# Kernel tuning notes

Hardware: AMD Instinct MI355X
Metric: run time of the kernel (lower is better)

The kernel has to match this reference:

```python
import math
import jax, jax.numpy as jnp
import numpy as np

# --- Cayley-Dickson octonion structure constants: e_i * e_j = sign * e_{i XOR j} ---
def _cd_tables(levels=3):
    idx = np.array([[0]]); sgn = np.array([[1]])
    for _ in range(levels):
        n = idx.shape[0]; N = 2 * n
        I = np.zeros((N, N), np.int64); S = np.zeros((N, N), np.int64)
        cj = lambda j: 1 if j == 0 else -1  # conj sign of basis element j
        for i in range(n):
            for j in range(n):
                I[i, j] = idx[i, j];             S[i, j] = sgn[i, j]
                I[i, n + j] = n + idx[j, i];     S[i, n + j] = sgn[j, i]
                I[n + i, j] = n + idx[i, j];     S[n + i, j] = sgn[i, j] * cj(j)
                I[n + i, n + j] = idx[j, i];     S[n + i, n + j] = -cj(j) * sgn[j, i]
        idx, sgn = I, S
    return idx, sgn

_OIDX, _OSGN = _cd_tables()
# Octonion-structured linear: out_i = sum_j SIGN[i,j] * x_j @ W[WIDX[i,j]], WIDX[i,j]=i^j
_WIDX = np.array([[i ^ j for j in range(8)] for i in range(8)], np.int64)
_SIGN = np.array([[_OSGN[j, i ^ j] for j in range(8)] for i in range(8)], np.float32)


def _oct_linear(x, W):
    # x: [B,T,C], W: [8, C/8, C/8]
    B, T, C = x.shape
    Cp = C // 8
    parts = x.reshape(B, T, 8, Cp)
    Weff = jnp.asarray(_SIGN)[:, :, None, None] * W[jnp.asarray(_WIDX)]  # [8,8,Cp,Cp]
    return jnp.einsum('btjp,ijpq->btiq', parts, Weff).reshape(B, T, C)


def _rope(x, cos, sin):
    # x: [B,T,H,D]; consecutive channel pairs form complex numbers
    B, T, H, D = x.shape
    xr = x.reshape(B, T, H, D // 2, 2)
    xe, xo = xr[..., 0], xr[..., 1]
    c = cos[None, :, None, :]
    s = sin[None, :, None, :]
    return jnp.stack([xe * c - xo * s, xe * s + xo * c], axis=-1).reshape(B, T, H, D)


def _forward(x, Wq, Wk, Wv, Wo, mixer_W, mixer_beta, freqs_cos, freqs_sin):
    B, T, C = x.shape
    H = 32; D = C // H
    q = _oct_linear(x, Wq).reshape(B, T, H, D)
    k = _oct_linear(x, Wk).reshape(B, T, H, D)
    v = _oct_linear(x, Wv).reshape(B, T, H, D)
    q = _rope(q, freqs_cos, freqs_sin)
    k = _rope(k, freqs_cos, freqs_sin)
    q = q.transpose(0, 2, 1, 3)  # [B,H,T,D]
    k = k.transpose(0, 2, 1, 3)
    v = v.transpose(0, 2, 1, 3)
    scores = jnp.einsum('bhqd,bhkd->bhqk', q, k) / jnp.sqrt(jnp.float32(D))
    mask = jnp.tril(jnp.ones((T, T), bool))
    scores = jnp.where(mask, scores, jnp.finfo(scores.dtype).min)
    y = jnp.einsum('bhqk,bhkd->bhqd', jax.nn.softmax(scores, axis=-1), v)  # [B,H,T,D]
    # octonion head mixing in groups of 8 heads
    G = H // 8
    yg = y.reshape(B, G, 8, T, D)
    Weff = jnp.asarray(_SIGN)[:, :, None, None] * mixer_W[jnp.asarray(_WIDX)]  # [8,8,D,D]
    mixed = jnp.einsum('bgjtd,ijde->bgite', yg, Weff) * mixer_beta
    y = mixed.reshape(B, H, T, D).transpose(0, 2, 1, 3).reshape(B, T, C)
    return _oct_linear(y, Wo)


def setup_inputs() -> dict:
    key = jax.random.key(0)
    ks = jax.random.split(key, 8)
    B, T, C, H = 1, 2048, 4096, 32
    D = C // H; Cp = C // 8
    x = jax.random.normal(ks[0], (B, T, C), jnp.float32)
    Wq = jax.random.normal(ks[1], (8, Cp, Cp), jnp.float32) * 0.02
    Wk = jax.random.normal(ks[2], (8, Cp, Cp), jnp.float32) * 0.02
    Wv = jax.random.normal(ks[3], (8, Cp, Cp), jnp.float32) * 0.02
    Wo = jax.random.normal(ks[4], (8, Cp, Cp), jnp.float32) * 0.02
    mixer_W = jax.random.normal(ks[5], (8, D, D), jnp.float32) * 0.02
    mixer_beta = jnp.ones((D,), jnp.float32) * np.float32(math.sqrt(3.0 / (2.0 * D)))
    half = D // 2
    inv = 1.0 / (10000.0 ** (np.arange(half) * 2.0 / D))
    ang = np.arange(T)[:, None] * inv[None, :]
    freqs_cos = jnp.asarray(np.cos(ang), jnp.float32)
    freqs_sin = jnp.asarray(np.sin(ang), jnp.float32)
    return dict(x=x, Wq=Wq, Wk=Wk, Wv=Wv, Wo=Wo, mixer_W=mixer_W,
                mixer_beta=mixer_beta, freqs_cos=freqs_cos, freqs_sin=freqs_sin)


def reference(x, Wq, Wk, Wv, Wo, mixer_W, mixer_beta, freqs_cos, freqs_sin):
    return _forward(x, Wq, Wk, Wv, Wo, mixer_W, mixer_beta, freqs_cos, freqs_sin)
```

## Files before the change

kernel.cpp:

```cpp
#include <hip/hip_runtime.h>

typedef float f32x4 __attribute__((ext_vector_type(4)));
typedef __bf16 bf16x8 __attribute__((ext_vector_type(8)));
typedef unsigned short u16;
typedef u16 u16x8 __attribute__((ext_vector_type(8)));

__constant__ float c_osgn[64] = {
  1, 1, 1, 1, 1, 1, 1, 1,
  1,-1, 1,-1, 1,-1,-1, 1,
  1,-1,-1, 1, 1, 1,-1,-1,
  1, 1,-1,-1, 1,-1, 1,-1,
  1,-1,-1,-1,-1, 1, 1, 1,
  1, 1,-1, 1,-1,-1,-1, 1,
  1, 1, 1,-1,-1, 1,-1,-1,
  1,-1, 1, 1,-1,-1, 1,-1
};

__device__ __forceinline__ u16 f2bf(float f) {
  union { float f; unsigned u; } v; v.f = f;
  unsigned u = v.u;
  return (u16)((u + 0x7fffu + ((u >> 16) & 1u)) >> 16);
}
__device__ __forceinline__ float bf2f(u16 h) {
  union { unsigned u; float f; } v; v.u = ((unsigned)h) << 16;
  return v.f;
}

typedef const __attribute__((address_space(1))) void* as1cv;
typedef __attribute__((address_space(3))) void* as3v;
__device__ __forceinline__ void load16_lds(const void* g, void* l) {
  __builtin_amdgcn_global_load_lds((as1cv)g, (as3v)l, 16, 0, 0);
}

__global__ void conv_f32_bf16_vec(const float* __restrict__ src, u16* __restrict__ dst) {
  int i = blockIdx.x * 256 + threadIdx.x;
  float4 v = ((const float4*)src)[i];
  ushort4 o; o.x = f2bf(v.x); o.y = f2bf(v.y); o.z = f2bf(v.z); o.w = f2bf(v.w);
  ((ushort4*)dst)[i] = o;
}

__global__ __launch_bounds__(256) void transpose_w2(const float* __restrict__ W,
                                                    u16* __restrict__ Wt) {
  __shared__ float t[64][65];
  const int w = blockIdx.z, p0 = blockIdx.y * 64, q0 = blockIdx.x * 64;
  const float* src = W + ((long)w * 512 + p0) * 512 + q0;
  const int tid = threadIdx.x;
  const int r = tid >> 2, c0 = (tid & 3) * 16;
#pragma unroll
  for (int j = 0; j < 4; j++) {
    float4 v = *(const float4*)(src + (long)r * 512 + c0 + j * 4);
    t[r][c0 + j * 4 + 0] = v.x; t[r][c0 + j * 4 + 1] = v.y;
    t[r][c0 + j * 4 + 2] = v.z; t[r][c0 + j * 4 + 3] = v.w;
  }
  __syncthreads();
  u16* dst = Wt + ((long)w * 512 + q0) * 512 + p0;
#pragma unroll
  for (int j = 0; j < 2; j++) {
    u16x8 o;
#pragma unroll
    for (int k = 0; k < 8; k++) o[k] = f2bf(t[c0 + j * 8 + k][r]);
    *(u16x8*)(dst + (long)r * 512 + c0 + j * 8) = o;
  }
}

__global__ void transpose_wm(const float* __restrict__ W, const float* __restrict__ beta,
                             u16* __restrict__ Wt) {
  int idx = blockIdx.x * 256 + threadIdx.x;
  int w = idx >> 14, rem = idx & 16383;
  int e = rem >> 7, d = rem & 127;
  Wt[(w << 14) + (e << 7) + d] = f2bf(W[(w << 14) + (d << 7) + e] * beta[e]);
}

template <typename OUT_T>
__global__ __launch_bounds__(512, 2) void oct_gemm2(
    const u16* __restrict__ A, const u16* __restrict__ WtB, OUT_T* __restrict__ Cout,
    int K, int lda, int ldo, long wslab, long oslab)
{
  __shared__ u16 As[2][256][64];
  __shared__ u16 Bs[2][128][64];
  const int NT = K >> 6;

  const int nwg = gridDim.x * gridDim.y;
  const int lin = blockIdx.y * gridDim.x + blockIdx.x;
  const int swz = (lin & 7) * (nwg >> 3) + (lin >> 3);
  const int bx = swz % gridDim.x, by = swz / gridDim.x;

  const int nglob = bx * 128;
  const int z = nglob >> 12;
  const int np = nglob & 4095;
  const int bi = np >> 9;
  const int nsub = np & 511;
  const int bm = by * 256;
  const u16* Wt = WtB + (long)z * wslab;
  OUT_T* outp = Cout + (long)z * oslab;

  const int tid = threadIdx.x;
  const int lane = tid & 63, w = tid >> 6;
  const int l15 = lane & 15, lg = lane >> 4;
  const int wm = w >> 1, wn = w & 1;
  const int srow = lane >> 3;
  const int sgr  = (lane & 7) ^ srow;

  f32x4 acc[4][4];
#pragma unroll
  for (int a = 0; a < 4; a++)
#pragma unroll
    for (int b = 0; b < 4; b++) acc[a][b] = f32x4{0.f, 0.f, 0.f, 0.f};

  auto stage = [&](int t, int buf) {
    const int k0 = t << 6;
    const int widx = bi ^ (k0 >> 9);
    const int kl = k0 & 511;
    const u16* Wsrc = Wt + (long)widx * 262144 + kl;
#pragma unroll
    for (int i = 0; i < 4; i++) {
      const int r = w * 32 + i * 8;
      const u16* g = A + (long)(bm + r + srow) * lda + k0 + sgr * 8;
      load16_lds(g, (void*)&As[buf][r][0]);
    }
#pragma unroll
    for (int i = 0; i < 2; i++) {
      const int r = w * 16 + i * 8;
      const u16* g = Wsrc + (long)(nsub + r + srow) * 512 + sgr * 8;
      load16_lds(g, (void*)&Bs[buf][r][0]);
    }
  };

  stage(0, 0);
  stage(1, 1);

  for (int t = 0; t < NT; ++t) {
    if (t == NT - 1) asm volatile("s_waitcnt vmcnt(0)" ::: "memory");
    else             asm volatile("s_waitcnt vmcnt(6)" ::: "memory");
    __builtin_amdgcn_s_barrier();
    asm volatile("" ::: "memory");

    const int cur = t & 1;
    const int bj = t >> 3;
    const unsigned xm = (c_osgn[bj * 8 + (bi ^ bj)] < 0.f) ? 0x80008000u : 0u;

#pragma unroll
    for (int kk = 0; kk < 64; kk += 32) {
      const int gsw = (((kk >> 3) + lg) ^ (l15 & 7)) * 8;
      uint4 a4[4];
      bf16x8 bF[4];
#pragma unroll
      for (int mt = 0; mt < 4; mt++)
        a4[mt] = *(const uint4*)&As[cur][wm * 64 + mt * 16 + l15][gsw];
      if (xm) {
#pragma unroll
        for (int mt = 0; mt < 4; mt++) {
          a4[mt].x ^= xm; a4[mt].y ^= xm; a4[mt].z ^= xm; a4[mt].w ^= xm;
        }
      }
#pragma unroll
      for (int nt = 0; nt < 4; nt++)
        bF[nt] = *(const bf16x8*)&Bs[cur][wn * 64 + nt * 16 + l15][gsw];
#pragma unroll
      for (int mt = 0; mt < 4; mt++)
#pragma unroll
        for (int nt = 0; nt < 4; nt++)
          acc[mt][nt] = __builtin_amdgcn_mfma_f32_16x16x32_bf16(
              *(const bf16x8*)&a4[mt], bF[nt], acc[mt][nt], 0, 0, 0);
    }

    asm volatile("" ::: "memory");
    __builtin_amdgcn_s_barrier();
    asm volatile("" ::: "memory");
    if (t + 2 < NT) stage(t + 2, cur);
  }

#pragma unroll
  for (int mt = 0; mt < 4; mt++)
#pragma unroll
    for (int nt = 0; nt < 4; nt++)
#pragma unroll
      for (int j = 0; j < 4; j++) {
        const int row = bm + wm * 64 + mt * 16 + 4 * lg + j;
        const int col = np + wn * 64 + nt * 16 + l15;
        const float v = acc[mt][nt][j];
        if constexpr (sizeof(OUT_T) == 2) outp[(long)row * ldo + col] = f2bf(v);
        else                              outp[(long)row * ldo + col] = v;
      }
}

template <typename OUT_T>
__global__ __launch_bounds__(256) void oct_gemm(
    const u16* __restrict__ A, const u16* __restrict__ Wt, OUT_T* __restrict__ Cout,
    int K, int lda, int ldo, int BS, long zA, long zW, long zC)
{
  A += blockIdx.z * zA;
  Wt += blockIdx.z * zW;
  Cout += blockIdx.z * zC;
  const int bm = blockIdx.y * 128, bn = blockIdx.x * 128;
  __shared__ u16 As[128][72];
  __shared__ u16 Bs[128][72];
  const int tid = threadIdx.x;
  const int lane = tid & 63, wid = tid >> 6;
  const int l15 = lane & 15, lg = lane >> 4;
  const int wm = (wid >> 1) * 64, wn = (wid & 1) * 64;
  f32x4 acc[4][4];
#pragma unroll
  for (int a = 0; a < 4; a++)
#pragma unroll
    for (int b = 0; b < 4; b++) acc[a][b] = f32x4{0.f, 0.f, 0.f, 0.f};

  const int bi = bn / BS;
  const int nsub = bn % BS;
  const int r = tid >> 3, kc = (tid & 7) * 8;

  for (int k0 = 0; k0 < K; k0 += 64) {
    const int bj = k0 / BS;
    const int w = bi ^ bj;
    const float sg = c_osgn[bj * 8 + w];
    const unsigned xm = (sg < 0.f) ? 0x80008000u : 0u;
    const u16* Wsrc = Wt + (long)w * BS * BS + (k0 % BS);
#pragma unroll
    for (int p = 0; p < 4; p++) {
      int row = p * 32 + r;
      uint4 va = *(const uint4*)(A + (long)(bm + row) * lda + k0 + kc);
      *(uint4*)&As[row][kc] = va;
      uint4 vb = *(const uint4*)(Wsrc + (long)(nsub + row) * BS + kc);
      vb.x ^= xm; vb.y ^= xm; vb.z ^= xm; vb.w ^= xm;
      *(uint4*)&Bs[row][kc] = vb;
    }
    __syncthreads();
#pragma unroll
    for (int kk = 0; kk < 64; kk += 32) {
      bf16x8 aF[4], bF[4];
#pragma unroll
      for (int mt = 0; mt < 4; mt++)
        aF[mt] = *(const bf16x8*)&As[wm + mt * 16 + l15][kk + 8 * lg];
#pragma unroll
      for (int nt = 0; nt < 4; nt++)
        bF[nt] = *(const bf16x8*)&Bs[wn + nt * 16 + l15][kk + 8 * lg];
#pragma unroll
      for (int mt = 0; mt < 4; mt++)
#pragma unroll
        for (int nt = 0; nt < 4; nt++)
          acc[mt][nt] = __builtin_amdgcn_mfma_f32_16x16x32_bf16(aF[mt], bF[nt], acc[mt][nt], 0, 0, 0);
    }
    __syncthreads();
  }
#pragma unroll
  for (int mt = 0; mt < 4; mt++)
#pragma unroll
    for (int nt = 0; nt < 4; nt++)
#pragma unroll
      for (int j = 0; j < 4; j++) {
        int row = bm + wm + mt * 16 + 4 * lg + j;
        int col = bn + wn + nt * 16 + l15;
        float v = acc[mt][nt][j];
        if constexpr (sizeof(OUT_T) == 2) Cout[(long)row * ldo + col] = f2bf(v);
        else                              Cout[(long)row * ldo + col] = v;
      }
}

__global__ void rope_qk(const u16* __restrict__ qg, const u16* __restrict__ kg,
                        const float* __restrict__ fc, const float* __restrict__ fs,
                        u16* __restrict__ qR, u16* __restrict__ kR)
{
  int idx = blockIdx.x * 256 + threadIdx.x;
  int t = idx >> 9, co = (idx & 511) << 3;
  int h = co >> 7, dl = co & 127, m0 = dl >> 1;
  float4 c4 = *(const float4*)(fc + t * 64 + m0);
  float4 s4 = *(const float4*)(fs + t * 64 + m0);
  float cc[4] = {c4.x, c4.y, c4.z, c4.w};
  float ss[4] = {s4.x, s4.y, s4.z, s4.w};
  long src = (long)t * 4096 + co;
  long dst = ((long)h * 2048 + t) * 128 + dl;
  u16x8 q8 = *(const u16x8*)(qg + src);
  u16x8 k8 = *(const u16x8*)(kg + src);
  u16x8 qo, ko;
#pragma unroll
  for (int p = 0; p < 4; p++) {
    float xe = bf2f(q8[2 * p]), xo = bf2f(q8[2 * p + 1]);
    qo[2 * p]     = f2bf(xe * cc[p] - xo * ss[p]);
    qo[2 * p + 1] = f2bf(xe * ss[p] + xo * cc[p]);
    float ye = bf2f(k8[2 * p]), yo = bf2f(k8[2 * p + 1]);
    ko[2 * p]     = f2bf(ye * cc[p] - yo * ss[p]);
    ko[2 * p + 1] = f2bf(ye * ss[p] + yo * cc[p]);
  }
  *(u16x8*)(qR + dst) = qo;
  *(u16x8*)(kR + dst) = ko;
}

__global__ void v_transpose(const u16* __restrict__ vg, u16* __restrict__ vT)
{
  int h = blockIdx.x, t0 = blockIdx.y * 64;
  __shared__ u16 lds[64][136];
  int tid = threadIdx.x;
  int rr = tid >> 4, ch = (tid & 15) * 8;
#pragma unroll
  for (int p = 0; p < 4; p++) {
    int row = p * 16 + rr;
    *(uint4*)&lds[row][ch] = *(const uint4*)(vg + (long)(t0 + row) * 4096 + h * 128 + ch);
  }
  __syncthreads();
  int dd = tid >> 3, tc = (tid & 7) * 8;
#pragma unroll
  for (int p = 0; p < 4; p++) {
    int d = p * 32 + dd;
    u16x8 o;
#pragma unroll
    for (int j = 0; j < 8; j++) o[j] = lds[tc + j][d];
    *(u16x8*)(vT + ((long)h * 128 + d) * 2048 + t0 + tc) = o;
  }
}

__global__ __launch_bounds__(256, 2) void attn3(
    const u16* __restrict__ qR, const u16* __restrict__ kR,
    const u16* __restrict__ vT, u16* __restrict__ y)
{
  const int bid = blockIdx.x;
  const int h = bid & 31;
  const int u = bid >> 5;
  const int qb = (u < 8) ? (u * 2) : (31 - u * 2);
  const int q0 = qb * 128;

  const int tid = threadIdx.x;
  const int lane = tid & 63, w = tid >> 6;
  const int l15 = lane & 15, lg = lane >> 4;

  __shared__ u16 Ks[2][64][128];
  __shared__ u16 Vs[2][128][64];
  __shared__ u16 Ps[4][32][64];

  auto stageK = [&](int kb, int buf) {
    const long kbase = (long)h * 2048 + (long)kb * 64;
#pragma unroll
    for (int i = 0; i < 4; i++) {
      const int j = w * 4 + i;
      const int row = j * 4 + (lane >> 4);
      const int sg = (lane & 15) ^ (row & 7);
      load16_lds(kR + (kbase + row) * 128 + sg * 8, (void*)&Ks[buf][j * 4][0]);
    }
  };
  auto stageV = [&](int kb, int buf) {
    const long vbase = (long)h * 128 * 2048 + (long)kb * 64;
#pragma unroll
    for (int i = 0; i < 4; i++) {
      const int j = w * 4 + i;
      const int row = j * 8 + (lane >> 3);
      const int sg = (lane & 7) ^ (row & 7);
      load16_lds(vT + vbase + (long)row * 2048 + sg * 8, (void*)&Vs[buf][j * 8][0]);
    }
  };

  stageK(0, 0);
  stageV(0, 0);

  bf16x8 aQ[2][4];
#pragma unroll
  for (int rs = 0; rs < 2; rs++) {
    const long qbase = ((long)h * 2048 + q0 + w * 32 + rs * 16 + l15) * 128;
#pragma unroll
    for (int c = 0; c < 4; c++)
      aQ[rs][c] = *(const bf16x8*)(qR + qbase + 32 * c + 8 * lg);
  }

  float m[2][4], lsum[2][4];
  f32x4 Y[2][8];
#pragma unroll
  for (int rs = 0; rs < 2; rs++)
#pragma unroll
    for (int rr = 0; rr < 4; rr++) { m[rs][rr] = -1e30f; lsum[rs][rr] = 0.f; }
#pragma unroll
  for (int rs = 0; rs < 2; rs++)
#pragma unroll
    for (int dt = 0; dt < 8; dt++) Y[rs][dt] = f32x4{0.f, 0.f, 0.f, 0.f};

  const float scale = 0.08838834764831845f;
  const int nkb = 2 * qb + 2;

  for (int kb = 0; kb < nkb; kb++) {
    const int buf = kb & 1;
    const int k0 = kb * 64;
    if (kb + 1 < nkb) { stageK(kb + 1, buf ^ 1); stageV(kb + 1, buf ^ 1); }
    if (kb + 1 < nkb) asm volatile("s_waitcnt vmcnt(8)" ::: "memory");
    else              asm volatile("s_waitcnt vmcnt(0)" ::: "memory");
    __builtin_amdgcn_s_barrier();
    asm volatile("" ::: "memory");

    f32x4 S[2][4];
#pragma unroll
    for (int rs = 0; rs < 2; rs++)
#pragma unroll
      for (int ks = 0; ks < 4; ks++) S[rs][ks] = f32x4{0.f, 0.f, 0.f, 0.f};
#pragma unroll
    for (int c = 0; c < 4; c++) {
      bf16x8 bK[4];
#pragma unroll
      for (int ks = 0; ks < 4; ks++)
        bK[ks] = *(const bf16x8*)&Ks[buf][ks * 16 + l15][(((4 * c + lg) ^ (l15 & 7)) * 8)];
#pragma unroll
      for (int rs = 0; rs < 2; rs++)
#pragma unroll
        for (int ks = 0; ks < 4; ks++)
          S[rs][ks] = __builtin_amdgcn_mfma_f32_16x16x32_bf16(aQ[rs][c], bK[ks], S[rs][ks], 0, 0, 0);
    }

#pragma unroll
    for (int rs = 0; rs < 2; rs++) {
      const int qrow0 = q0 + w * 32 + rs * 16 + 4 * lg;
#pragma unroll
      for (int ks = 0; ks < 4; ks++) {
        const int kg = k0 + ks * 16 + l15;
#pragma unroll
        for (int rr = 0; rr < 4; rr++) {
          float s = S[rs][ks][rr] * scale;
          S[rs][ks][rr] = (kg > qrow0 + rr) ? -1e30f : s;
        }
      }
      float sf[4];
      bool need = false;
#pragma unroll
      for (int rr = 0; rr < 4; rr++) {
        float mx = fmaxf(fmaxf(S[rs][0][rr], S[rs][1][rr]),
                         fmaxf(S[rs][2][rr], S[rs][3][rr]));
#pragma unroll
        for (int off = 1; off < 16; off <<= 1) mx = fmaxf(mx, __shfl_xor(mx, off));
        const bool upd = (mx > m[rs][rr] + 8.f);
        const float mn = upd ? mx : m[rs][rr];
        const float sc = upd ? __expf(m[rs][rr] - mn) : 1.f;
        need |= upd;
        m[rs][rr] = mn;
        float rsum = 0.f;
#pragma unroll
        for (int ks = 0; ks < 4; ks++) {
          float e = __expf(S[rs][ks][rr] - mn);
          S[rs][ks][rr] = e;
          rsum += e;
        }
#pragma unroll
        for (int off = 1; off < 16; off <<= 1) rsum += __shfl_xor(rsum, off);
        lsum[rs][rr] = lsum[rs][rr] * sc + rsum;
        sf[rr] = sc;
      }
      if (__any(need)) {
#pragma unroll
        for (int dt = 0; dt < 8; dt++) {
          f32x4 yv = Y[rs][dt];
          yv[0] *= sf[0]; yv[1] *= sf[1]; yv[2] *= sf[2]; yv[3] *= sf[3];
          Y[rs][dt] = yv;
        }
      }
#pragma unroll
      for (int ks = 0; ks < 4; ks++)
#pragma unroll
        for (int rr = 0; rr < 4; rr++) {
          const int row = rs * 16 + 4 * lg + rr;
          const int G = (2 * ks + (l15 >> 3)) ^ (row & 7);
          Ps[w][row][G * 8 + (l15 & 7)] = f2bf(S[rs][ks][rr]);
        }
    }

#pragma unroll
    for (int kk = 0; kk < 2; kk++) {
      const int pg = ((4 * kk + lg) ^ (l15 & 7)) * 8;
      bf16x8 pF0 = *(const bf16x8*)&Ps[w][l15][pg];
      bf16x8 pF1 = *(const bf16x8*)&Ps[w][16 + l15][pg];
#pragma unroll
      for (int dt = 0; dt < 8; dt++) {
        bf16x8 vF = *(const bf16x8*)&Vs[buf][dt * 16 + l15][pg];
        Y[0][dt] = __builtin_amdgcn_mfma_f32_16x16x32_bf16(pF0, vF, Y[0][dt], 0, 0, 0);
        Y[1][dt] = __builtin_amdgcn_mfma_f32_16x16x32_bf16(pF1, vF, Y[1][dt], 0, 0, 0);
      }
    }
    asm volatile("" ::: "memory");
    __builtin_amdgcn_s_barrier();
    asm volatile("" ::: "memory");
  }

#pragma unroll
  for (int rs = 0; rs < 2; rs++) {
    float inv[4];
#pragma unroll
    for (int rr = 0; rr < 4; rr++) inv[rr] = 1.0f / lsum[rs][rr];
#pragma unroll
    for (int dt = 0; dt < 8; dt++)
#pragma unroll
      for (int rr = 0; rr < 4; rr++)
        y[(long)(q0 + w * 32 + rs * 16 + 4 * lg + rr) * 4096 + h * 128 + dt * 16 + l15] =
            f2bf(Y[rs][dt][rr] * inv[rr]);
  }
}

extern "C" void kernel_launch(void* const* d_in, const int* in_sizes, int n_in,
                              void* d_out, int out_size, void* d_ws, size_t ws_size,
                              hipStream_t stream) {
  const float* x    = (const float*)d_in[0];
  const float* Wq   = (const float*)d_in[1];
  const float* Wk   = (const float*)d_in[2];
  const float* Wv   = (const float*)d_in[3];
  const float* Wo   = (const float*)d_in[4];
  const float* Wm   = (const float*)d_in[5];
  const float* beta = (const float*)d_in[6];
  const float* fc   = (const float*)d_in[7];
  const float* fs   = (const float*)d_in[8];
  float* out = (float*)d_out;

  const long TC = 2048L * 4096L;
  const long WSZ = 8L * 512 * 512;
  u16* ws  = (u16*)d_ws;
  u16* xb  = ws;
  u16* wt  = ws + TC;
  u16* wmt = wt + 4 * WSZ;
  u16* g3  = wmt + 131072L;
  u16* r3  = g3 + 3 * TC;
  u16* yatt = xb;
  u16* ymix = g3;

  conv_f32_bf16_vec<<<TC / 4 / 256, 256, 0, stream>>>(x, xb);
  transpose_w2<<<dim3(8, 8, 8), 256, 0, stream>>>(Wq, wt + 0 * WSZ);
  transpose_w2<<<dim3(8, 8, 8), 256, 0, stream>>>(Wk, wt + 1 * WSZ);
  transpose_w2<<<dim3(8, 8, 8), 256, 0, stream>>>(Wv, wt + 2 * WSZ);
  transpose_w2<<<dim3(8, 8, 8), 256, 0, stream>>>(Wo, wt + 3 * WSZ);
  transpose_wm<<<512, 256, 0, stream>>>(Wm, beta, wmt);

  oct_gemm2<u16><<<dim3(96, 8), 512, 0, stream>>>(
      xb, wt, g3, 4096, 4096, 4096, WSZ, TC);

  rope_qk<<<TC / 8 / 256, 256, 0, stream>>>(g3, g3 + TC, fc, fs, r3, r3 + TC);
  v_transpose<<<dim3(32, 32), 256, 0, stream>>>(g3 + 2 * TC, r3 + 2 * TC);

  attn3<<<512, 256, 0, stream>>>(r3, r3 + TC, r3 + 2 * TC, yatt);

  oct_gemm<u16><<<dim3(8, 16, 4), 256, 0, stream>>>(
      yatt, wmt, ymix, 1024, 4096, 4096, 128, 1024L, 0L, 1024L);

  oct_gemm2<float><<<dim3(32, 8), 512, 0, stream>>>(
      ymix, wt + 3 * WSZ, out, 4096, 4096, 4096, 0L, 0L);
}
```

Measured before the change: 489.3 us.

## Fuse RoPE into QKV GEMM epilogue and route mixer GEMM through pipelined kernel

The QKV octonion GEMM now applies rotary embedding in its epilogue, using a lane shuffle to pair even and odd channels. It writes Q and K straight into head-major layout, which removes the separate rope_qk kernel and its read and write of Q and K. The head-mixer GEMM switches from the older unpipelined oct_gemm to the generalized double-buffered oct_gemm2f, with the block size and slab parameterized. The trade-off is strided epilogue stores and per-element cos/sin loads inside the GEMM, and the mixer GEMM now runs fewer, larger tiles.

```diff
diff --git a/kernel.cpp b/kernel.cpp
--- a/kernel.cpp
+++ b/kernel.cpp
@@ -71,14 +71,19 @@
   Wt[(w << 14) + (e << 7) + d] = f2bf(W[(w << 14) + (d << 7) + e] * beta[e]);
 }
 
-template <typename OUT_T>
-__global__ __launch_bounds__(512, 2) void oct_gemm2(
-    const u16* __restrict__ A, const u16* __restrict__ WtB, OUT_T* __restrict__ Cout,
-    int K, int lda, int ldo, long wslab, long oslab)
+template <int MODE>
+__global__ __launch_bounds__(512, 2) void oct_gemm2f(
+    const u16* __restrict__ A, const u16* __restrict__ WtB,
+    void* __restrict__ out0, void* __restrict__ out1, void* __restrict__ out2,
+    const float* __restrict__ fc, const float* __restrict__ fs,
+    int K, int lda, int ldo,
+    int slab_shift, int bs_shift, long wslab, long oslab, long acolslab)
 {
   __shared__ u16 As[2][256][64];
   __shared__ u16 Bs[2][128][64];
   const int NT = K >> 6;
+  const int BS = 1 << bs_shift;
+  const long wblk = (long)BS * BS;
 
   const int nwg = gridDim.x * gridDim.y;
   const int lin = blockIdx.y * gridDim.x + blockIdx.x;
@@ -86,13 +91,13 @@
   const int bx = swz % gridDim.x, by = swz / gridDim.x;
 
   const int nglob = bx * 128;
-  const int z = nglob >> 12;
-  const int np = nglob & 4095;
-  const int bi = np >> 9;
-  const int nsub = np & 511;
+  const int z = nglob >> slab_shift;
+  const int np = nglob & ((1 << slab_shift) - 1);
+  const int bi = np >> bs_shift;
+  const int nsub = np & (BS - 1);
   const int bm = by * 256;
   const u16* Wt = WtB + (long)z * wslab;
-  OUT_T* outp = Cout + (long)z * oslab;
+  const long acol0 = (long)z * acolslab;
 
   const int tid = threadIdx.x;
   const int lane = tid & 63, w = tid >> 6;
@@ -109,19 +114,19 @@
 
   auto stage = [&](int t, int buf) {
     const int k0 = t << 6;
-    const int widx = bi ^ (k0 >> 9);
-    const int kl = k0 & 511;
-    const u16* Wsrc = Wt + (long)widx * 262144 + kl;
+    const int widx = bi ^ (k0 >> bs_shift);
+    const int kl = k0 & (BS - 1);
+    const u16* Wsrc = Wt + (long)widx * wblk + kl;
 #pragma unroll
     for (int i = 0; i < 4; i++) {
       const int r = w * 32 + i * 8;
-      const u16* g = A + (long)(bm + r + srow) * lda + k0 + sgr * 8;
+      const u16* g = A + (long)(bm + r + srow) * lda + acol0 + k0 + sgr * 8;
       load16_lds(g, (void*)&As[buf][r][0]);
     }
 #pragma unroll
     for (int i = 0; i < 2; i++) {
       const int r = w * 16 + i * 8;
-      const u16* g = Wsrc + (long)(nsub + r + srow) * 512 + sgr * 8;
+      const u16* g = Wsrc + (long)(nsub + r + srow) * BS + sgr * 8;
       load16_lds(g, (void*)&Bs[buf][r][0]);
     }
   };
@@ -130,13 +135,13 @@
   stage(1, 1);
 
   for (int t = 0; t < NT; ++t) {
-    if (t == NT - 1) asm volatile("s_waitcnt vmcnt(0)" ::: "memory");
-    else             asm volatile("s_waitcnt vmcnt(6)" ::: "memory");
+    if (t + 1 < NT) asm volatile("s_waitcnt vmcnt(6)" ::: "memory");
+    else            asm volatile("s_waitcnt vmcnt(0)" ::: "memory");
     __builtin_amdgcn_s_barrier();
     asm volatile("" ::: "memory");
 
     const int cur = t & 1;
-    const int bj = t >> 3;
+    const int bj = t >> (bs_shift - 6);
     const unsigned xm = (c_osgn[bj * 8 + (bi ^ bj)] < 0.f) ? 0x80008000u : 0u;
 
 #pragma unroll
@@ -170,119 +175,57 @@
     if (t + 2 < NT) stage(t + 2, cur);
   }
 
-#pragma unroll
-  for (int mt = 0; mt < 4; mt++)
-#pragma unroll
-    for (int nt = 0; nt < 4; nt++)
-#pragma unroll
-      for (int j = 0; j < 4; j++) {
-        const int row = bm + wm * 64 + mt * 16 + 4 * lg + j;
-        const int col = np + wn * 64 + nt * 16 + l15;
-        const float v = acc[mt][nt][j];
-        if constexpr (sizeof(OUT_T) == 2) outp[(long)row * ldo + col] = f2bf(v);
-        else                              outp[(long)row * ldo + col] = v;
-      }
-}
-
-template <typename OUT_T>
-__global__ __launch_bounds__(256) void oct_gemm(
-    const u16* __restrict__ A, const u16* __restrict__ Wt, OUT_T* __restrict__ Cout,
-    int K, int lda, int ldo, int BS, long zA, long zW, long zC)
-{
-  A += blockIdx.z * zA;
-  Wt += blockIdx.z * zW;
-  Cout += blockIdx.z * zC;
-  const int bm = blockIdx.y * 128, bn = blockIdx.x * 128;
-  __shared__ u16 As[128][72];
-  __shared__ u16 Bs[128][72];
-  const int tid = threadIdx.x;
-  const int lane = tid & 63, wid = tid >> 6;
-  const int l15 = lane & 15, lg = lane >> 4;
-  const int wm = (wid >> 1) * 64, wn = (wid & 1) * 64;
-  f32x4 acc[4][4];
-#pragma unroll
-  for (int a = 0; a < 4; a++)
-#pragma unroll
-    for (int b = 0; b < 4; b++) acc[a][b] = f32x4{0.f, 0.f, 0.f, 0.f};
-
-  const int bi = bn / BS;
-  const int nsub = bn % BS;
-  const int r = tid >> 3, kc = (tid & 7) * 8;
-
-  for (int k0 = 0; k0 < K; k0 += 64) {
-    const int bj = k0 / BS;
-    const int w = bi ^ bj;
-    const float sg = c_osgn[bj * 8 + w];
-    const unsigned xm = (sg < 0.f) ? 0x80008000u : 0u;
-    const u16* Wsrc = Wt + (long)w * BS * BS + (k0 % BS);
-#pragma unroll
-    for (int p = 0; p < 4; p++) {
-      int row = p * 32 + r;
-      uint4 va = *(const uint4*)(A + (long)(bm + row) * lda + k0 + kc);
-      *(uint4*)&As[row][kc] = va;
-      uint4 vb = *(const uint4*)(Wsrc + (long)(nsub + row) * BS + kc);
-      vb.x ^= xm; vb.y ^= xm; vb.z ^= xm; vb.w ^= xm;
-      *(uint4*)&Bs[row][kc] = vb;
-    }
-    __syncthreads();
-#pragma unroll
-    for (int kk = 0; kk < 64; kk += 32) {
-      bf16x8 aF[4], bF[4];
+  if constexpr (MODE == 1) {
+    if (z == 2) {
+      u16* vg = (u16*)out2;
 #pragma unroll
       for (int mt = 0; mt < 4; mt++)
-        aF[mt] = *(const bf16x8*)&As[wm + mt * 16 + l15][kk + 8 * lg];
+#pragma unroll
+        for (int nt = 0; nt < 4; nt++)
+#pragma unroll
+          for (int j = 0; j < 4; j++) {
+            const int row = bm + wm * 64 + mt * 16 + 4 * lg + j;
+            const int col = np + wn * 64 + nt * 16 + l15;
+            vg[(long)row * 4096 + col] = f2bf(acc[mt][nt][j]);
+          }
+    } else {
+      u16* dq = (u16*)(z == 0 ? out0 : out1);
+      const int h = np >> 7;
+#pragma unroll
+      for (int mt = 0; mt < 4; mt++)
+#pragma unroll
+        for (int nt = 0; nt < 4; nt++) {
+          const int d = wn * 64 + nt * 16 + l15;
+          const int p = d >> 1;
+          const bool ev = (l15 & 1) == 0;
+#pragma unroll
+          for (int j = 0; j < 4; j++) {
+            const int trow = bm + wm * 64 + mt * 16 + 4 * lg + j;
+            const float v = acc[mt][nt][j];
+            const float sh = __shfl_xor(v, 1);
+            const float c = fc[trow * 64 + p];
+            const float s = fs[trow * 64 + p];
+            const float o = ev ? (v * c - sh * s) : (sh * s + v * c);
+            dq[((long)h * 2048 + trow) * 128 + d] = f2bf(o);
+          }
+        }
+    }
+  } else {
+#pragma unroll
+    for (int mt = 0; mt < 4; mt++)
 #pragma unroll
       for (int nt = 0; nt < 4; nt++)
-        bF[nt] = *(const bf16x8*)&Bs[wn + nt * 16 + l15][kk + 8 * lg];
-#pragma unroll
-      for (int mt = 0; mt < 4; mt++)
-#pragma unroll
-        for (int nt = 0; nt < 4; nt++)
-          acc[mt][nt] = __builtin_amdgcn_mfma_f32_16x16x32_bf16(aF[mt], bF[nt], acc[mt][nt], 0, 0, 0);
-    }
-    __syncthreads();
-  }
-#pragma unroll
-  for (int mt = 0; mt < 4; mt++)
-#pragma unroll
-    for (int nt = 0; nt < 4; nt++)
-#pragma unroll
-      for (int j = 0; j < 4; j++) {
-        int row = bm + wm + mt * 16 + 4 * lg + j;
-        int col = bn + wn + nt * 16 + l15;
-        float v = acc[mt][nt][j];
-        if constexpr (sizeof(OUT_T) == 2) Cout[(long)row * ldo + col] = f2bf(v);
-        else                              Cout[(long)row * ldo + col] = v;
-      }
-}
-
-__global__ void rope_qk(const u16* __restrict__ qg, const u16* __restrict__ kg,
-                        const float* __restrict__ fc, const float* __restrict__ fs,
-                        u16* __restrict__ qR, u16* __restrict__ kR)
-{
-  int idx = blockIdx.x * 256 + threadIdx.x;
-  int t = idx >> 9, co = (idx & 511) << 3;
-  int h = co >> 7, dl = co & 127, m0 = dl >> 1;
-  float4 c4 = *(const float4*)(fc + t * 64 + m0);
-  float4 s4 = *(const float4*)(fs + t * 64 + m0);
-  float cc[4] = {c4.x, c4.y, c4.z, c4.w};
-  float ss[4] = {s4.x, s4.y, s4.z, s4.w};
-  long src = (long)t * 4096 + co;
-  long dst = ((long)h * 2048 + t) * 128 + dl;
-  u16x8 q8 = *(const u16x8*)(qg + src);
-  u16x8 k8 = *(const u16x8*)(kg + src);
-  u16x8 qo, ko;
-#pragma unroll
-  for (int p = 0; p < 4; p++) {
-    float xe = bf2f(q8[2 * p]), xo = bf2f(q8[2 * p + 1]);
-    qo[2 * p]     = f2bf(xe * cc[p] - xo * ss[p]);
-    qo[2 * p + 1] = f2bf(xe * ss[p] + xo * cc[p]);
-    float ye = bf2f(k8[2 * p]), yo = bf2f(k8[2 * p + 1]);
-    ko[2 * p]     = f2bf(ye * cc[p] - yo * ss[p]);
-    ko[2 * p + 1] = f2bf(ye * ss[p] + yo * cc[p]);
-  }
-  *(u16x8*)(qR + dst) = qo;
-  *(u16x8*)(kR + dst) = ko;
+#pragma unroll
+        for (int j = 0; j < 4; j++) {
+          const int row = bm + wm * 64 + mt * 16 + 4 * lg + j;
+          const int col = np + wn * 64 + nt * 16 + l15;
+          const float v = acc[mt][nt][j];
+          if constexpr (MODE == 0)
+            ((u16*)out0)[(long)z * oslab + (long)row * ldo + col] = f2bf(v);
+          else
+            ((float*)out0)[(long)row * ldo + col] = v;
+        }
+  }
 }
 
 __global__ void v_transpose(const u16* __restrict__ vg, u16* __restrict__ vT)
@@ -518,17 +461,19 @@
   transpose_w2<<<dim3(8, 8, 8), 256, 0, stream>>>(Wo, wt + 3 * WSZ);
   transpose_wm<<<512, 256, 0, stream>>>(Wm, beta, wmt);
 
-  oct_gemm2<u16><<<dim3(96, 8), 512, 0, stream>>>(
-      xb, wt, g3, 4096, 4096, 4096, WSZ, TC);
-
-  rope_qk<<<TC / 8 / 256, 256, 0, stream>>>(g3, g3 + TC, fc, fs, r3, r3 + TC);
-  v_transpose<<<dim3(32, 32), 256, 0, stream>>>(g3 + 2 * TC, r3 + 2 * TC);
+  oct_gemm2f<1><<<dim3(96, 8), 512, 0, stream>>>(
+      xb, wt, (void*)r3, (void*)(r3 + TC), (void*)g3, fc, fs,
+      4096, 4096, 4096, 12, 9, WSZ, 0L, 0L);
+
+  v_transpose<<<dim3(32, 32), 256, 0, stream>>>(g3, r3 + 2 * TC);
 
   attn3<<<512, 256, 0, stream>>>(r3, r3 + TC, r3 + 2 * TC, yatt);
 
-  oct_gemm<u16><<<dim3(8, 16, 4), 256, 0, stream>>>(
-      yatt, wmt, ymix, 1024, 4096, 4096, 128, 1024L, 0L, 1024L);
-
-  oct_gemm2<float><<<dim3(32, 8), 512, 0, stream>>>(
-      ymix, wt + 3 * WSZ, out, 4096, 4096, 4096, 0L, 0L);
-}
+  oct_gemm2f<0><<<dim3(32, 8), 512, 0, stream>>>(
+      yatt, wmt, (void*)ymix, nullptr, nullptr, nullptr, nullptr,
+      1024, 4096, 4096, 10, 7, 0L, 1024L, 1024L);
+
+  oct_gemm2f<2><<<dim3(32, 8), 512, 0, stream>>>(
+      ymix, wt + 3 * WSZ, (void*)out, nullptr, nullptr, nullptr, nullptr,
+      4096, 4096, 4096, 12, 9, 0L, 0L, 0L);
+}
```

New measurement: 486.0 us. About the same (-0.7%).
